# Kernel optimization log

Hardware: AMD Instinct MI355X
Metric: run time of the kernel (lower is better)

Reference implementation:

```python
import jax, jax.numpy as jnp
import numpy as np

EMBED = 1024
HEAD = 64
B, S = 4, 4096

def setup_inputs() -> dict:
    key = jax.random.key(0)
    k1, k2, k3, k4, k5, k6 = jax.random.split(key, 6)
    scale = 1.0 / np.sqrt(EMBED)
    return {
        "query": jax.random.normal(k1, (B, S, EMBED), dtype=jnp.float32),
        "key": jax.random.normal(k2, (B, S, EMBED), dtype=jnp.float32),
        "value": jax.random.normal(k3, (B, S, EMBED), dtype=jnp.float32),
        "wq": jax.random.normal(k4, (EMBED, HEAD), dtype=jnp.float32) * scale,
        "wk": jax.random.normal(k5, (EMBED, HEAD), dtype=jnp.float32) * scale,
        "wv": jax.random.normal(k6, (EMBED, HEAD), dtype=jnp.float32) * scale,
    }

def reference(query, key, value, wq, wk, wv):
    # projections (bias-free linears)
    q = query @ wq            # [B,S,H]
    k = key @ wk              # [B,S,H]
    v = value @ wv            # [B,S,H]
    scores = jnp.einsum('bqh,bkh->bqk', q, k) / jnp.sqrt(jnp.float32(HEAD))
    S_len = scores.shape[-1]
    causal = jnp.tril(jnp.ones((S_len, S_len), dtype=bool))
    scores = jnp.where(causal, scores, -jnp.inf)
    attn = jax.nn.softmax(scores, axis=-1)
    return attn @ v           # [B,S,H]
```

## Files before the change

kernel.cpp:

```cpp
#include <hip/hip_runtime.h>
#include <hip/hip_bf16.h>

#define EMBED 1024
#define HEAD 64
#define SEQ 4096

typedef __attribute__((ext_vector_type(8))) short short8;
typedef __attribute__((ext_vector_type(4))) float f32x4;

union S8u { short8 v; uint u[4]; ushort s[8]; };
union U4f { uint4 q; float f[4]; };

__device__ __forceinline__ ushort f2bf(float f) {
  union { float f; uint u; } x; x.f = f;
  return (ushort)((x.u + 0x7fffu + ((x.u >> 16) & 1u)) >> 16);
}

__device__ __forceinline__ ushort f2bf_n(float f) {
  union { __hip_bfloat16 h; ushort u; } cv;
  cv.h = __float2bfloat16(f);
  return cv.u;
}

__device__ __forceinline__ short8 ld16(const ushort* p) {
  uint4 q = *(const uint4*)p;
  S8u t; t.u[0] = q.x; t.u[1] = q.y; t.u[2] = q.z; t.u[3] = q.w;
  return t.v;
}

__global__ __launch_bounds__(256) void prep_w(const float* __restrict__ wq,
                                              const float* __restrict__ wk,
                                              const float* __restrict__ wv,
                                              ushort* __restrict__ wT) {
  int idx = blockIdx.x * 256 + threadIdx.x;
  if (idx >= 3 * HEAD * EMBED) return;
  int t = idx >> 16;
  int rem = idx & 0xFFFF;
  int c = rem >> 10;
  int k = rem & 1023;
  const float* w = (t == 0) ? wq : (t == 1) ? wk : wv;
  wT[idx] = f2bf_n(w[k * HEAD + c]);
}

__global__ __launch_bounds__(256, 3) void proj_kernel(
    const float* __restrict__ qsrc, const float* __restrict__ ksrc,
    const float* __restrict__ vsrc, const ushort* __restrict__ wT,
    ushort* __restrict__ qb, ushort* __restrict__ kb, ushort* __restrict__ vt) {
  __shared__ __align__(16) char smem[24576];

  const int t = blockIdx.y;
  const float* src = (t == 0) ? qsrc : (t == 1) ? ksrc : vsrc;
  const ushort* wt = wT + t * (HEAD * EMBED);
  const int tid = threadIdx.x;
  const int lane = tid & 63;
  const int wid = tid >> 6;
  const int c = lane & 15;
  const int g = lane >> 4;
  const int row0 = blockIdx.x * 64;
  const int phase = (blockIdx.x + 5 * blockIdx.y) & 15;

  const float* gA = src + (size_t)(row0 + (tid >> 4)) * EMBED + (tid & 15) * 4;
  const ushort* gB = wt + (size_t)(tid >> 3) * EMBED + (tid & 7) * 8;
  const int wA = (tid >> 4) * 256 + (((tid & 15) * 16) ^ (((tid >> 4) & 7) << 4));
  const int wB = 16384 + (tid >> 3) * 128 + (((tid & 7) * 16) ^ (((tid >> 3) & 7) << 4));

  const int rA = (wid * 16 + c) * 256;
  const int swc = (c & 7) << 4;

  f32x4 acc[4];
#pragma unroll
  for (int i = 0; i < 4; ++i) acc[i] = {0.f, 0.f, 0.f, 0.f};

  uint4 sA0, sA1, sA2, sA3, sB0, sB1;
  {
    const int ki = phase * 64;
    sA0 = *(const uint4*)(gA + ki);
    sA1 = *(const uint4*)(gA + 16384 + ki);
    sA2 = *(const uint4*)(gA + 32768 + ki);
    sA3 = *(const uint4*)(gA + 49152 + ki);
    sB0 = *(const uint4*)(gB + ki);
    sB1 = *(const uint4*)(gB + 32768 + ki);
  }

  for (int r = 0; r < 16; ++r) {
    *(uint4*)(smem + wA)         = sA0;
    *(uint4*)(smem + wA + 4096)  = sA1;
    *(uint4*)(smem + wA + 8192)  = sA2;
    *(uint4*)(smem + wA + 12288) = sA3;
    *(uint4*)(smem + wB)         = sB0;
    *(uint4*)(smem + wB + 4096)  = sB1;
    __syncthreads();

    if (r + 1 < 16) {
      const int ki = (((r + 1 + phase) & 15)) * 64;
      sA0 = *(const uint4*)(gA + ki);
      sA1 = *(const uint4*)(gA + 16384 + ki);
      sA2 = *(const uint4*)(gA + 32768 + ki);
      sA3 = *(const uint4*)(gA + 49152 + ki);
      sB0 = *(const uint4*)(gB + ki);
      sB1 = *(const uint4*)(gB + 32768 + ki);
    }

#pragma unroll
    for (int s = 0; s < 2; ++s) {
      U4f af0, af1;
      af0.q = *(const uint4*)(smem + rA + ((128 * s + 32 * g) ^ swc));
      af1.q = *(const uint4*)(smem + rA + ((128 * s + 32 * g + 16) ^ swc));
      S8u a;
      a.s[0] = f2bf_n(af0.f[0]); a.s[1] = f2bf_n(af0.f[1]);
      a.s[2] = f2bf_n(af0.f[2]); a.s[3] = f2bf_n(af0.f[3]);
      a.s[4] = f2bf_n(af1.f[0]); a.s[5] = f2bf_n(af1.f[1]);
      a.s[6] = f2bf_n(af1.f[2]); a.s[7] = f2bf_n(af1.f[3]);
#pragma unroll
      for (int nf = 0; nf < 4; ++nf) {
        uint4 bq = *(const uint4*)(smem + 16384 + (16 * nf + c) * 128 + ((64 * s + 16 * g) ^ swc));
        S8u b; b.u[0] = bq.x; b.u[1] = bq.y; b.u[2] = bq.z; b.u[3] = bq.w;
        acc[nf] = __builtin_amdgcn_mfma_f32_16x16x32_bf16(a.v, b.v, acc[nf], 0, 0, 0);
      }
    }
    __syncthreads();
  }

  if (t == 2) {
    ushort (*vtile)[72] = (ushort(*)[72])smem;
#pragma unroll
    for (int nf = 0; nf < 4; ++nf)
#pragma unroll
      for (int rr = 0; rr < 4; ++rr)
        vtile[nf * 16 + c][wid * 16 + 4 * g + rr] = f2bf_n(acc[nf][rr]);
    __syncthreads();
    int d = tid >> 2;
    int s0 = (tid & 3) << 4;
    int bb = row0 >> 12;
    int sbase = row0 & (SEQ - 1);
    ushort* dst = vt + ((size_t)(bb * HEAD + d) << 12) + sbase + s0;
    const uint4* srcp = (const uint4*)&vtile[d][s0];
    *(uint4*)dst = srcp[0];
    *(uint4*)(dst + 8) = srcp[1];
  } else {
    int row_base = row0 + wid * 16 + 4 * g;
    float scale = (t == 0) ? 0.18033688011112042f : 1.0f;
    ushort* dstb = (t == 0) ? qb : kb;
#pragma unroll
    for (int nf = 0; nf < 4; ++nf)
#pragma unroll
      for (int rr = 0; rr < 4; ++rr)
        dstb[(size_t)(row_base + rr) * HEAD + nf * 16 + c] = f2bf_n(acc[nf][rr] * scale);
  }
}

__global__ __launch_bounds__(512, 2) void flash_kernel(
    const ushort* __restrict__ qb, const ushort* __restrict__ kb,
    const ushort* __restrict__ vt, float* __restrict__ Opart,
    float* __restrict__ mlpart) {
  __shared__ __align__(16) char smem[16384];

  const int tid = threadIdx.x;
  const int lane = tid & 63;
  const int w = tid >> 6;
  const int c = lane & 15, g = lane >> 4;

  const int bid = blockIdx.x;
  const int band = 15 - (bid >> 4);
  const int b = (bid >> 2) & 3;
  const int j = bid & 3;
  const int ck = band + 1;
  const int kt0 = j * ck;
  const int q0w = band * 256 + w * 32;

  const int srow = tid >> 3;
  const int scol = (tid & 7) << 4;
  const int sdst = srow * 128 + (scol ^ ((srow & 7) << 4));
  const char* kgp = (const char*)(kb + (size_t)b * SEQ * HEAD) + (size_t)kt0 * 8192 + tid * 16;
  const char* vgp = (const char*)(vt + (size_t)b * HEAD * SEQ) + (size_t)srow * 8192 + kt0 * 128 + scol;

  short8 qa[2][2];
#pragma unroll
  for (int qf = 0; qf < 2; ++qf) {
    const ushort* qrow = qb + (size_t)(b * SEQ + q0w + 16 * qf + c) * HEAD + 8 * g;
    qa[qf][0] = ld16(qrow);
    qa[qf][1] = ld16(qrow + 32);
  }

  f32x4 O[4][2];
#pragma unroll
  for (int i = 0; i < 4; ++i)
#pragma unroll
    for (int qf = 0; qf < 2; ++qf) O[i][qf] = {0.f, 0.f, 0.f, 0.f};
  float m[2] = {-1e30f, -1e30f};
  float l[2] = {0.f, 0.f};

  uint4 sK = *(const uint4*)kgp;
  uint4 sV = *(const uint4*)vgp;

  for (int r = 0; r < ck; ++r) {
    *(uint4*)(smem + sdst) = sK;
    *(uint4*)(smem + 8192 + sdst) = sV;
    __syncthreads();

    if (r + 1 < ck) {
      kgp += 8192; vgp += 128;
      sK = *(const uint4*)kgp;
      sV = *(const uint4*)vgp;
    }

    const int kt = kt0 + r;
    const int k0 = kt << 6;
    if (k0 <= q0w + 31) {
      f32x4 Sf[4][2];
#pragma unroll
      for (int i = 0; i < 4; ++i)
#pragma unroll
        for (int qf = 0; qf < 2; ++qf) Sf[i][qf] = {0.f, 0.f, 0.f, 0.f};
#pragma unroll
      for (int nf = 0; nf < 4; ++nf) {
        int row = 16 * nf + c;
        int sw = (row & 7) << 4;
        uint4 kv = *(const uint4*)(smem + row * 128 + ((16 * g) ^ sw));
        S8u ka0;
        ka0.u[0] = kv.x; ka0.u[1] = kv.y; ka0.u[2] = kv.z; ka0.u[3] = kv.w;
#pragma unroll
        for (int qf = 0; qf < 2; ++qf)
          Sf[nf][qf] = __builtin_amdgcn_mfma_f32_16x16x32_bf16(ka0.v, qa[qf][0], Sf[nf][qf], 0, 0, 0);
        uint4 kv2 = *(const uint4*)(smem + row * 128 + ((64 + 16 * g) ^ sw));
        S8u ka1;
        ka1.u[0] = kv2.x; ka1.u[1] = kv2.y; ka1.u[2] = kv2.z; ka1.u[3] = kv2.w;
#pragma unroll
        for (int qf = 0; qf < 2; ++qf)
          Sf[nf][qf] = __builtin_amdgcn_mfma_f32_16x16x32_bf16(ka1.v, qa[qf][1], Sf[nf][qf], 0, 0, 0);
      }

      if (k0 + 63 > q0w) {
#pragma unroll
        for (int nf = 0; nf < 4; ++nf)
#pragma unroll
          for (int qf = 0; qf < 2; ++qf)
#pragma unroll
            for (int rr = 0; rr < 4; ++rr)
              if (k0 + nf * 16 + 4 * g + rr > q0w + 16 * qf + c) Sf[nf][qf][rr] = -1e30f;
      }

#pragma unroll
      for (int qf = 0; qf < 2; ++qf) {
        float x0 = fmaxf(fmaxf(Sf[0][qf][0], Sf[0][qf][1]), fmaxf(Sf[0][qf][2], Sf[0][qf][3]));
        float x1 = fmaxf(fmaxf(Sf[1][qf][0], Sf[1][qf][1]), fmaxf(Sf[1][qf][2], Sf[1][qf][3]));
        float x2 = fmaxf(fmaxf(Sf[2][qf][0], Sf[2][qf][1]), fmaxf(Sf[2][qf][2], Sf[2][qf][3]));
        float x3 = fmaxf(fmaxf(Sf[3][qf][0], Sf[3][qf][1]), fmaxf(Sf[3][qf][2], Sf[3][qf][3]));
        float rm = fmaxf(fmaxf(x0, x1), fmaxf(x2, x3));
        rm = fmaxf(rm, __shfl_xor(rm, 16));
        rm = fmaxf(rm, __shfl_xor(rm, 32));
        rm = fmaxf(rm, m[qf]);
        float alpha = exp2f(m[qf] - rm);
        m[qf] = rm;
#pragma unroll
        for (int nf = 0; nf < 4; ++nf)
#pragma unroll
          for (int rr = 0; rr < 4; ++rr)
            Sf[nf][qf][rr] = exp2f(Sf[nf][qf][rr] - rm);
        float s0 = (Sf[0][qf][0] + Sf[0][qf][1]) + (Sf[0][qf][2] + Sf[0][qf][3]);
        float s1 = (Sf[1][qf][0] + Sf[1][qf][1]) + (Sf[1][qf][2] + Sf[1][qf][3]);
        float s2 = (Sf[2][qf][0] + Sf[2][qf][1]) + (Sf[2][qf][2] + Sf[2][qf][3]);
        float s3 = (Sf[3][qf][0] + Sf[3][qf][1]) + (Sf[3][qf][2] + Sf[3][qf][3]);
        float rs = (s0 + s1) + (s2 + s3);
        rs += __shfl_xor(rs, 16);
        rs += __shfl_xor(rs, 32);
        l[qf] = l[qf] * alpha + rs;
#pragma unroll
        for (int nf = 0; nf < 4; ++nf)
#pragma unroll
          for (int rr = 0; rr < 4; ++rr)
            O[nf][qf][rr] *= alpha;

#pragma unroll
        for (int sl = 0; sl < 2; ++sl) {
          S8u pa;
#pragma unroll
          for (int rr = 0; rr < 4; ++rr) {
            pa.s[rr]     = f2bf(Sf[2 * sl][qf][rr]);
            pa.s[rr + 4] = f2bf(Sf[2 * sl + 1][qf][rr]);
          }
#pragma unroll
          for (int nf = 0; nf < 4; ++nf) {
            int row = 16 * nf + c;
            int sw = (row & 7) << 4;
            S8u vbf;
            uint2 lo = *(const uint2*)(smem + 8192 + row * 128 + ((64 * sl + 8 * g) ^ sw));
            uint2 hi = *(const uint2*)(smem + 8192 + row * 128 + ((64 * sl + 32 + 8 * g) ^ sw));
            vbf.u[0] = lo.x; vbf.u[1] = lo.y; vbf.u[2] = hi.x; vbf.u[3] = hi.y;
            O[nf][qf] = __builtin_amdgcn_mfma_f32_16x16x32_bf16(vbf.v, pa.v, O[nf][qf], 0, 0, 0);
          }
        }
      }
    }
    __syncthreads();
  }

  const size_t pi = (size_t)((b * 16 + band) * 4 + j);
#pragma unroll
  for (int qf = 0; qf < 2; ++qf) {
    int ql = w * 32 + 16 * qf + c;
#pragma unroll
    for (int nf = 0; nf < 4; ++nf)
      *(f32x4*)&Opart[pi * 16384 + (size_t)ql * 64 + 16 * nf + 4 * g] = O[nf][qf];
    if (g == 0) {
      mlpart[pi * 512 + ql * 2]     = m[qf];
      mlpart[pi * 512 + ql * 2 + 1] = l[qf];
    }
  }
}

__global__ __launch_bounds__(256) void merge_kernel(const float* __restrict__ Opart,
                                                    const float* __restrict__ mlpart,
                                                    float* __restrict__ out) {
  int i = blockIdx.x * 256 + threadIdx.x;
  int dq = i & 15;
  int row = i >> 4;
  int b = row >> 12;
  int qrow = row & 4095;
  int band = qrow >> 8;
  int q = qrow & 255;
  size_t pi0 = (size_t)((b * 16 + band) * 4);

  float mm[4], M = -1e30f;
#pragma unroll
  for (int jj = 0; jj < 4; ++jj) { mm[jj] = mlpart[(pi0 + jj) * 512 + q * 2]; M = fmaxf(M, mm[jj]); }
  float wgt[4], L = 0.f;
#pragma unroll
  for (int jj = 0; jj < 4; ++jj) {
    wgt[jj] = exp2f(mm[jj] - M);
    L += wgt[jj] * mlpart[(pi0 + jj) * 512 + q * 2 + 1];
  }
  f32x4 acc = {0.f, 0.f, 0.f, 0.f};
#pragma unroll
  for (int jj = 0; jj < 4; ++jj) {
    f32x4 t = *(const f32x4*)&Opart[(pi0 + jj) * 16384 + (size_t)q * 64 + 4 * dq];
#pragma unroll
    for (int rr = 0; rr < 4; ++rr) acc[rr] += wgt[jj] * t[rr];
  }
  float inv = 1.0f / L;
  f32x4 res;
#pragma unroll
  for (int rr = 0; rr < 4; ++rr) res[rr] = acc[rr] * inv;
  *(f32x4*)&out[(size_t)row * HEAD + 4 * dq] = res;
}

extern "C" void kernel_launch(void* const* d_in, const int* in_sizes, int n_in,
                              void* d_out, int out_size, void* d_ws, size_t ws_size,
                              hipStream_t stream) {
  const float* qsrc = (const float*)d_in[0];
  const float* ksrc = (const float*)d_in[1];
  const float* vsrc = (const float*)d_in[2];
  const float* wq = (const float*)d_in[3];
  const float* wk = (const float*)d_in[4];
  const float* wv = (const float*)d_in[5];
  float* out = (float*)d_out;

  char* ws = (char*)d_ws;
  ushort* wT = (ushort*)ws;
  ushort* qb = (ushort*)(ws + 393216);
  ushort* kb = (ushort*)(ws + 393216 + 2097152);
  ushort* vt = (ushort*)(ws + 393216 + 2 * 2097152);
  float* Opart = (float*)(ws + 393216 + 3 * 2097152);
  float* mlpart = (float*)(ws + 393216 + 3 * 2097152 + 16777216);

  prep_w<<<dim3(768), dim3(256), 0, stream>>>(wq, wk, wv, wT);
  proj_kernel<<<dim3(256, 3), dim3(256), 0, stream>>>(qsrc, ksrc, vsrc, wT, qb, kb, vt);
  flash_kernel<<<dim3(256), dim3(512), 0, stream>>>(qb, kb, vt, Opart, mlpart);
  merge_kernel<<<dim3(1024), dim3(256), 0, stream>>>(Opart, mlpart, out);
}
```

Baseline: 87.52 us.

## Split projection K dimension across two blocks and add combine kernel

The projection GEMM is split along the embedding (reduction) dimension into two halves via a new grid z dimension, doubling the block count from 768 to 1536 for better occupancy. Each half writes fp32 partial results to a workspace buffer that aliases the Opart region. A new combine kernel sums the two partials, applies the Q scale, converts to bf16 and does the V transpose. This adds an extra launch and extra fp32 global traffic (partials write and read) in exchange for more parallelism in the bandwidth-bound projection.

Result: slower. 97.51 us (+11.4%).

```diff
diff --git a/kernel.cpp b/kernel.cpp
--- a/kernel.cpp
+++ b/kernel.cpp
@@ -45,10 +45,11 @@
 __global__ __launch_bounds__(256, 3) void proj_kernel(
     const float* __restrict__ qsrc, const float* __restrict__ ksrc,
     const float* __restrict__ vsrc, const ushort* __restrict__ wT,
-    ushort* __restrict__ qb, ushort* __restrict__ kb, ushort* __restrict__ vt) {
+    float* __restrict__ Ppart) {
   __shared__ __align__(16) char smem[24576];
 
   const int t = blockIdx.y;
+  const int kz = blockIdx.z;
   const float* src = (t == 0) ? qsrc : (t == 1) ? ksrc : vsrc;
   const ushort* wt = wT + t * (HEAD * EMBED);
   const int tid = threadIdx.x;
@@ -57,7 +58,7 @@
   const int c = lane & 15;
   const int g = lane >> 4;
   const int row0 = blockIdx.x * 64;
-  const int phase = (blockIdx.x + 5 * blockIdx.y) & 15;
+  const int phase = (blockIdx.x + 5 * blockIdx.y) & 7;
 
   const float* gA = src + (size_t)(row0 + (tid >> 4)) * EMBED + (tid & 15) * 4;
   const ushort* gB = wt + (size_t)(tid >> 3) * EMBED + (tid & 7) * 8;
@@ -73,7 +74,7 @@
 
   uint4 sA0, sA1, sA2, sA3, sB0, sB1;
   {
-    const int ki = phase * 64;
+    const int ki = (kz * 8 + phase) * 64;
     sA0 = *(const uint4*)(gA + ki);
     sA1 = *(const uint4*)(gA + 16384 + ki);
     sA2 = *(const uint4*)(gA + 32768 + ki);
@@ -82,7 +83,7 @@
     sB1 = *(const uint4*)(gB + 32768 + ki);
   }
 
-  for (int r = 0; r < 16; ++r) {
+  for (int r = 0; r < 8; ++r) {
     *(uint4*)(smem + wA)         = sA0;
     *(uint4*)(smem + wA + 4096)  = sA1;
     *(uint4*)(smem + wA + 8192)  = sA2;
@@ -91,8 +92,8 @@
     *(uint4*)(smem + wB + 4096)  = sB1;
     __syncthreads();
 
-    if (r + 1 < 16) {
-      const int ki = (((r + 1 + phase) & 15)) * 64;
+    if (r + 1 < 8) {
+      const int ki = (kz * 8 + ((r + 1 + phase) & 7)) * 64;
       sA0 = *(const uint4*)(gA + ki);
       sA1 = *(const uint4*)(gA + 16384 + ki);
       sA2 = *(const uint4*)(gA + 32768 + ki);
@@ -121,31 +122,58 @@
     __syncthreads();
   }
 
-  if (t == 2) {
-    ushort (*vtile)[72] = (ushort(*)[72])smem;
-#pragma unroll
-    for (int nf = 0; nf < 4; ++nf)
-#pragma unroll
-      for (int rr = 0; rr < 4; ++rr)
-        vtile[nf * 16 + c][wid * 16 + 4 * g + rr] = f2bf_n(acc[nf][rr]);
+  float* pp = Ppart + ((size_t)(t * 2 + kz) * 16384 + row0) * 64;
+  const int rb = wid * 16 + 4 * g;
+#pragma unroll
+  for (int nf = 0; nf < 4; ++nf)
+#pragma unroll
+    for (int rr = 0; rr < 4; ++rr)
+      pp[(rb + rr) * 64 + nf * 16 + c] = acc[nf][rr];
+}
+
+__global__ __launch_bounds__(256) void combine_kernel(
+    const float* __restrict__ Ppart, ushort* __restrict__ qb,
+    ushort* __restrict__ kb, ushort* __restrict__ vt) {
+  __shared__ ushort vtile[64][72];
+  const int t = blockIdx.y;
+  const int row0 = blockIdx.x * 64;
+  const int tid = threadIdx.x;
+  const float* p0 = Ppart + ((size_t)(t * 2 + 0) * 16384 + row0) * 64;
+  const float* p1 = Ppart + ((size_t)(t * 2 + 1) * 16384 + row0) * 64;
+
+  if (t < 2) {
+    const float scale = (t == 0) ? 0.18033688011112042f : 1.0f;
+    ushort* dst = ((t == 0) ? qb : kb) + (size_t)row0 * 64;
+#pragma unroll
+    for (int j = 0; j < 4; ++j) {
+      int f4 = tid + j * 256;
+      f32x4 a = *(const f32x4*)(p0 + f4 * 4);
+      f32x4 b = *(const f32x4*)(p1 + f4 * 4);
+      ushort o[4];
+#pragma unroll
+      for (int e = 0; e < 4; ++e) o[e] = f2bf_n((a[e] + b[e]) * scale);
+      *(uint2*)(dst + f4 * 4) = *(const uint2*)o;
+    }
+  } else {
+    const int r = tid >> 2;
+    const int cc = (tid & 3) * 16;
+#pragma unroll
+    for (int j = 0; j < 4; ++j) {
+      f32x4 a = *(const f32x4*)(p0 + r * 64 + cc + j * 4);
+      f32x4 b = *(const f32x4*)(p1 + r * 64 + cc + j * 4);
+#pragma unroll
+      for (int e = 0; e < 4; ++e)
+        vtile[cc + j * 4 + e][r] = f2bf_n(a[e] + b[e]);
+    }
     __syncthreads();
     int d = tid >> 2;
     int s0 = (tid & 3) << 4;
     int bb = row0 >> 12;
     int sbase = row0 & (SEQ - 1);
-    ushort* dst = vt + ((size_t)(bb * HEAD + d) << 12) + sbase + s0;
+    ushort* dstv = vt + ((size_t)(bb * HEAD + d) << 12) + sbase + s0;
     const uint4* srcp = (const uint4*)&vtile[d][s0];
-    *(uint4*)dst = srcp[0];
-    *(uint4*)(dst + 8) = srcp[1];
-  } else {
-    int row_base = row0 + wid * 16 + 4 * g;
-    float scale = (t == 0) ? 0.18033688011112042f : 1.0f;
-    ushort* dstb = (t == 0) ? qb : kb;
-#pragma unroll
-    for (int nf = 0; nf < 4; ++nf)
-#pragma unroll
-      for (int rr = 0; rr < 4; ++rr)
-        dstb[(size_t)(row_base + rr) * HEAD + nf * 16 + c] = f2bf_n(acc[nf][rr] * scale);
+    *(uint4*)dstv = srcp[0];
+    *(uint4*)(dstv + 8) = srcp[1];
   }
 }
 
@@ -360,11 +388,13 @@
   ushort* qb = (ushort*)(ws + 393216);
   ushort* kb = (ushort*)(ws + 393216 + 2097152);
   ushort* vt = (ushort*)(ws + 393216 + 2 * 2097152);
+  float* Ppart = (float*)(ws + 393216 + 3 * 2097152);
   float* Opart = (float*)(ws + 393216 + 3 * 2097152);
   float* mlpart = (float*)(ws + 393216 + 3 * 2097152 + 16777216);
 
   prep_w<<<dim3(768), dim3(256), 0, stream>>>(wq, wk, wv, wT);
-  proj_kernel<<<dim3(256, 3), dim3(256), 0, stream>>>(qsrc, ksrc, vsrc, wT, qb, kb, vt);
+  proj_kernel<<<dim3(256, 3, 2), dim3(256), 0, stream>>>(qsrc, ksrc, vsrc, wT, Ppart);
+  combine_kernel<<<dim3(256, 3), dim3(256), 0, stream>>>(Ppart, qb, kb, vt);
   flash_kernel<<<dim3(256), dim3(512), 0, stream>>>(qb, kb, vt, Opart, mlpart);
   merge_kernel<<<dim3(1024), dim3(256), 0, stream>>>(Opart, mlpart, out);
 }
```
